# Kernel tuning notes

Hardware: AMD Instinct MI355X
Metric: run time of the kernel (lower is better)

Reference implementation:

```python
import jax, jax.numpy as jnp
import numpy as np

B, S, D_MODEL = 2, 2048, 512
KEY_DIM, VALUE_DIM, OUTPUT_DIM, NUM_HEADS = 256, 256, 512, 8


def setup_inputs() -> dict:
    key = jax.random.key(0)
    ks = jax.random.split(key, 12)
    s = 0.02
    return {
        "V": jax.random.normal(ks[0], (B, S, D_MODEL), jnp.float32),
        "Q": jax.random.normal(ks[1], (B, S, D_MODEL), jnp.float32),
        "K": jax.random.normal(ks[2], (B, S, D_MODEL), jnp.float32),
        "mask": jax.random.normal(ks[3], (B, 1, S, S), jnp.float32),
        "Wq": jax.random.normal(ks[4], (D_MODEL, KEY_DIM), jnp.float32) * s,
        "bq": jnp.zeros((KEY_DIM,), jnp.float32),
        "Wk": jax.random.normal(ks[5], (D_MODEL, KEY_DIM), jnp.float32) * s,
        "bk": jnp.zeros((KEY_DIM,), jnp.float32),
        "Wv": jax.random.normal(ks[6], (D_MODEL, VALUE_DIM), jnp.float32) * s,
        "bv": jnp.zeros((VALUE_DIM,), jnp.float32),
        "Wo": jax.random.normal(ks[7], (VALUE_DIM, OUTPUT_DIM), jnp.float32) * s,
        "bo": jnp.zeros((OUTPUT_DIM,), jnp.float32),
    }


def _split_heads(x, num_heads):
    # [B, S, H*d] -> [B, H, S, d]
    b, s, hd = x.shape
    return x.reshape(b, s, num_heads, hd // num_heads).transpose(0, 2, 1, 3)


def reference(V, Q, K, mask, Wq, bq, Wk, bk, Wv, bv, Wo, bo):
    denom = jnp.sqrt(jnp.float32(KEY_DIM))  # NOTE: full key_dim, as in source
    q = _split_heads(Q @ Wq + bq, NUM_HEADS)  # [B,H,S,dk]
    k = _split_heads(K @ Wk + bk, NUM_HEADS)
    scores = jnp.einsum("bhqd,bhkd->bhqk", q, k) / denom
    scores = scores + mask  # soft (additive) mask
    weights = jax.nn.softmax(scores, axis=-1)
    v = _split_heads(V @ Wv + bv, NUM_HEADS)  # [B,H,S,dv]
    ctx = jnp.einsum("bhqk,bhkd->bhqd", weights, v)  # [B,H,S,dv]
    b, h, s, d = ctx.shape
    ctx = ctx.transpose(0, 2, 1, 3).reshape(b, s, h * d)  # merge heads
    return ctx @ Wo + bo
```

## Files before the change

kernel.cpp:

```cpp
#include <hip/hip_runtime.h>

typedef __attribute__((ext_vector_type(8))) short bf16x8;
typedef __attribute__((ext_vector_type(4))) float f32x4;
typedef __attribute__((ext_vector_type(16))) float f32x16;

#define B_  2
#define S_  2048
#define DM  512
#define KD  256
#define HD  32
#define NH  8

__device__ __forceinline__ float bf2f(ushort u) {
    return __uint_as_float(((uint)u) << 16);
}
__device__ __forceinline__ ushort f2bf(float f) {
    uint x = __float_as_uint(f);
    return (ushort)((x + 0x7fffu + ((x >> 16) & 1u)) >> 16);
}
__device__ __forceinline__ uint cvt_pk_bf16(float lo, float hi) {
    uint r;
    asm("v_cvt_pk_bf16_f32 %0, %1, %2" : "=v"(r) : "v"(lo), "v"(hi));
    return r;
}
#define MFMA __builtin_amdgcn_mfma_f32_16x16x32_bf16
#define MFMA32 __builtin_amdgcn_mfma_f32_32x32x16_bf16

__device__ __forceinline__ int detect_isbf(const ushort* __restrict__ q)
{
    int lane = threadIdx.x & 63;
    int e = (q[lane] >> 7) & 0xFF;
    unsigned long long m = __ballot(e >= 100 && e <= 133);
    return __popcll(m) >= 58;
}

__global__ __launch_bounds__(256) void transpose_w(
    const void* __restrict__ Wq, const void* __restrict__ Wk, const void* __restrict__ Wv,
    const void* __restrict__ Wo,
    const void* __restrict__ bq, const void* __restrict__ bk,
    const void* __restrict__ bv, const void* __restrict__ bo,
    const ushort* __restrict__ qsrc,
    ushort* __restrict__ Wt, ushort* __restrict__ Wot, float* __restrict__ biasf)
{
    int isbf = detect_isbf(qsrc);
    int bid = blockIdx.x;
    if (bid >= 512) {
        for (int i = threadIdx.x; i < 1280; i += 256) {
            const void* bp; int off;
            if (i < 256)      { bp = bq; off = i; }
            else if (i < 512) { bp = bk; off = i - 256; }
            else if (i < 768) { bp = bv; off = i - 512; }
            else              { bp = bo; off = i - 768; }
            biasf[i] = isbf ? bf2f(((const ushort*)bp)[off]) : ((const float*)bp)[off];
        }
        return;
    }
    const void* W; int R, C; ushort* T;
    int m = bid >> 7, tix = bid & 127;
    if (m < 3) { W = (m == 0) ? Wq : (m == 1) ? Wk : Wv; R = 512; C = 256; T = Wt + m * 131072; }
    else       { W = Wo; R = 256; C = 512; T = Wot; }
    int tilesPerRow = C >> 5;
    int r0 = (tix / tilesPerRow) * 32, c0 = (tix % tilesPerRow) * 32;
    __shared__ float lds[32][33];
    int t = threadIdx.x;
    int rr = t >> 3, cc = (t & 7) * 4;
    if (isbf) {
        const ushort* Ws = (const ushort*)W;
        #pragma unroll
        for (int j = 0; j < 4; ++j) lds[rr][cc + j] = bf2f(Ws[(size_t)(r0 + rr) * C + c0 + cc + j]);
    } else {
        float4 v = *(const float4*)((const float*)W + (size_t)(r0 + rr) * C + c0 + cc);
        lds[rr][cc + 0] = v.x; lds[rr][cc + 1] = v.y; lds[rr][cc + 2] = v.z; lds[rr][cc + 3] = v.w;
    }
    __syncthreads();
    ushort4 o;
    o.x = f2bf(lds[cc + 0][rr]); o.y = f2bf(lds[cc + 1][rr]);
    o.z = f2bf(lds[cc + 2][rr]); o.w = f2bf(lds[cc + 3][rr]);
    int n = c0 + rr, k = r0 + cc;
    *(ushort4*)(T + ((((size_t)(n >> 4) * (R >> 3) + (k >> 3)) * 16 + (n & 15)) << 3) + (k & 7)) = o;
}

__global__ __launch_bounds__(256) void qkv_gemm(
    const void* __restrict__ Q, const void* __restrict__ K, const void* __restrict__ V,
    const ushort* __restrict__ Wt, const float* __restrict__ biasf,
    ushort* __restrict__ qh, ushort* __restrict__ kh, ushort* __restrict__ vT)
{
    int isbf = detect_isbf((const ushort*)Q);
    int y = blockIdx.y;
    const void* X = (y == 0) ? Q : (y == 1) ? K : V;
    int wave = threadIdx.x >> 6, lane = threadIdx.x & 63;
    int l16 = lane & 15, quad = lane >> 4;
    int m0 = blockIdx.x * 16;
    int n0 = wave * 64;
    const ushort* W = Wt + (size_t)y * (256 * 512);

    auto loadA = [&](int ks, bf16x8* a) {
        if (isbf) {
            *a = *(const bf16x8*)((const ushort*)X + (size_t)(m0 + l16) * 512 + ks + quad * 8);
        } else {
            const float* p = (const float*)X + (size_t)(m0 + l16) * 512 + ks + quad * 8;
            float4 f0 = *(const float4*)p, f1 = *(const float4*)(p + 4);
            union { uint u[4]; bf16x8 v; } cv;
            cv.u[0] = cvt_pk_bf16(f0.x, f0.y);
            cv.u[1] = cvt_pk_bf16(f0.z, f0.w);
            cv.u[2] = cvt_pk_bf16(f1.x, f1.y);
            cv.u[3] = cvt_pk_bf16(f1.z, f1.w);
            *a = cv.v;
        }
    };
    auto loadB = [&](int ks, bf16x8* b) {
        #pragma unroll
        for (int j = 0; j < 4; ++j)
            b[j] = *(const bf16x8*)(W + (((size_t)((n0 >> 4) + j) * 64 + (ks >> 3) + quad) * 16 + l16) * 8);
    };

    f32x4 acc[4] = {};
    bf16x8 aC, bC[4], aN, bN[4];
    loadA(0, &aC); loadB(0, bC);
    for (int ks = 0; ks < 512; ks += 32) {
        if (ks + 32 < 512) { loadA(ks + 32, &aN); loadB(ks + 32, bN); }
        #pragma unroll
        for (int j = 0; j < 4; ++j)
            acc[j] = MFMA(aC, bC[j], acc[j], 0, 0, 0);
        aC = aN;
        #pragma unroll
        for (int j = 0; j < 4; ++j) bC[j] = bN[j];
    }
    if (y < 2) {
        ushort* out = (y == 0) ? qh : kh;
        #pragma unroll
        for (int j = 0; j < 4; ++j) {
            int n = n0 + 16 * j + l16;
            float bs = biasf[y * 256 + n];
            int h = n >> 5, d = n & 31;
            #pragma unroll
            for (int r = 0; r < 4; ++r) {
                int rg = m0 + quad * 4 + r;
                int bb = rg >> 11, ss = rg & 2047;
                out[((((size_t)bb * NH + h) * S_ + ss) << 5) + d] = f2bf(acc[j][r] + bs);
            }
        }
    } else {
        int rg0 = m0 + quad * 4;
        int bb = rg0 >> 11, s0 = rg0 & 2047;
        #pragma unroll
        for (int j = 0; j < 4; ++j) {
            int n = n0 + 16 * j + l16;
            float bs = biasf[2 * 256 + n];
            int h = n >> 5, d = n & 31;
            ushort4 o;
            o.x = f2bf(acc[j][0] + bs); o.y = f2bf(acc[j][1] + bs);
            o.z = f2bf(acc[j][2] + bs); o.w = f2bf(acc[j][3] + bs);
            *(ushort4*)(vT + (((size_t)(bb * NH + h) * HD + d) * S_) + s0) = o;
        }
    }
}

__global__ __launch_bounds__(256) void attn(
    const ushort* __restrict__ qh, const ushort* __restrict__ kh,
    const ushort* __restrict__ vT, const void* __restrict__ maskp,
    float* __restrict__ pO, float* __restrict__ pl)
{
    __shared__ float ldsM[4][2][32][33];
    int isbf;
    {
        int lane = threadIdx.x & 63;
        ushort u = ((const ushort*)maskp)[lane];
        int e = (u >> 7) & 0xFF;
        unsigned long long m = __ballot(e >= 100 && e <= 133);
        isbf = __popcll(m) >= 58;
    }
    int wave = threadIdx.x >> 6, lane = threadIdx.x & 63;
    int l31 = lane & 31, hi = lane >> 5;
    int wid = blockIdx.x * 4 + wave;
    int chunk = wid & 1, qt32 = (wid >> 1) & 63, bh = wid >> 7;
    int b = bh >> 3;
    int q0 = qt32 * 32;
    const ushort* qb = qh + (size_t)bh * S_ * HD;
    const ushort* kb = kh + (size_t)bh * S_ * HD;
    const ushort* vb = vT + (size_t)bh * HD * S_;
    const ushort* mbb = (const ushort*)maskp + (size_t)b * S_ * S_;
    const float*  mbf = (const float*)maskp  + (size_t)b * S_ * S_;

    bf16x8 bq0 = *(const bf16x8*)(qb + (size_t)(q0 + l31) * HD + hi * 8);
    bf16x8 bq1 = *(const bf16x8*)(qb + (size_t)(q0 + l31) * HD + 16 + hi * 8);

    f32x16 O = {0,0,0,0,0,0,0,0,0,0,0,0,0,0,0,0};
    const f32x16 Z = {0,0,0,0,0,0,0,0,0,0,0,0,0,0,0,0};
    float lsum = 0.0f;

    int srow = (lane >> 3) & 7, scol = (lane & 7) * 4;
    float4 g[4];

    auto loadMg = [&](int k0) {
        if (isbf) {
            #pragma unroll
            for (int i = 0; i < 4; ++i) {
                ushort4 u = *(const ushort4*)(mbb + (size_t)(q0 + i * 8 + srow) * S_ + k0 + scol);
                float4 f; f.x = bf2f(u.x); f.y = bf2f(u.y); f.z = bf2f(u.z); f.w = bf2f(u.w);
                g[i] = f;
            }
        } else {
            #pragma unroll
            for (int i = 0; i < 4; ++i)
                g[i] = *(const float4*)(mbf + (size_t)(q0 + i * 8 + srow) * S_ + k0 + scol);
        }
    };
    auto writeM = [&](int buf) {
        #pragma unroll
        for (int i = 0; i < 4; ++i) {
            ldsM[wave][buf][i * 8 + srow][scol + 0] = g[i].x;
            ldsM[wave][buf][i * 8 + srow][scol + 1] = g[i].y;
            ldsM[wave][buf][i * 8 + srow][scol + 2] = g[i].z;
            ldsM[wave][buf][i * 8 + srow][scol + 3] = g[i].w;
        }
    };
    auto loadK = [&](int k0, bf16x8* K2) {
        K2[0] = *(const bf16x8*)(kb + (size_t)(k0 + l31) * HD + hi * 8);
        K2[1] = *(const bf16x8*)(kb + (size_t)(k0 + l31) * HD + 16 + hi * 8);
    };
    auto loadV = [&](int k0, bf16x8* V2) {
        V2[0] = *(const bf16x8*)(vb + (size_t)l31 * S_ + k0 + hi * 8);
        V2[1] = *(const bf16x8*)(vb + (size_t)l31 * S_ + k0 + 16 + hi * 8);
    };

    int kbase = chunk * 1024;

    auto sub = [&](int buf, bf16x8* Kc, bf16x8* Vc, bf16x8* Kn, bf16x8* Vn, int t) {
        float Mreg[16];
        #pragma unroll
        for (int r = 0; r < 16; ++r)
            Mreg[r] = ldsM[wave][buf][l31][(r & 3) + ((r >> 2) << 3) + (hi << 2)];
        int ktn = kbase + ((t + 1 < 32) ? (t + 1) : 31) * 32;
        loadK(ktn, Kn); loadV(ktn, Vn);
        f32x16 S = MFMA32(Kc[0], bq0, Z, 0, 0, 0);
        S = MFMA32(Kc[1], bq1, S, 0, 0, 0);
        writeM(buf ^ 1);
        int ktn2 = kbase + ((t + 2 < 32) ? (t + 2) : 31) * 32;
        loadMg(ktn2);
        float p[16];
        #pragma unroll
        for (int r = 0; r < 16; ++r) {
            p[r] = __expf(fmaf(S[r], 0.0625f, Mreg[r]));
            lsum += p[r];
        }
        union { uint u[4]; bf16x8 v; } pa0, pa1;
        {
            uint u0 = cvt_pk_bf16(p[0], p[1]),  w0 = cvt_pk_bf16(p[4], p[5]);
            uint u1 = cvt_pk_bf16(p[2], p[3]),  w1 = cvt_pk_bf16(p[6], p[7]);
            asm volatile("v_permlane32_swap_b32 %0, %1" : "+v"(u0), "+v"(w0));
            asm volatile("v_permlane32_swap_b32 %0, %1" : "+v"(u1), "+v"(w1));
            pa0.u[0] = u0; pa0.u[1] = u1; pa0.u[2] = w0; pa0.u[3] = w1;
            uint u2 = cvt_pk_bf16(p[8], p[9]),   w2 = cvt_pk_bf16(p[12], p[13]);
            uint u3 = cvt_pk_bf16(p[10], p[11]), w3 = cvt_pk_bf16(p[14], p[15]);
            asm volatile("v_permlane32_swap_b32 %0, %1" : "+v"(u2), "+v"(w2));
            asm volatile("v_permlane32_swap_b32 %0, %1" : "+v"(u3), "+v"(w3));
            pa1.u[0] = u2; pa1.u[1] = u3; pa1.u[2] = w2; pa1.u[3] = w3;
        }
        O = MFMA32(pa0.v, Vc[0], O, 0, 0, 0);
        O = MFMA32(pa1.v, Vc[1], O, 0, 0, 0);
    };

    bf16x8 KA[2], VA[2], KB[2], VB[2];
    loadK(kbase, KA); loadV(kbase, VA);
    loadMg(kbase); writeM(0);
    loadMg(kbase + 32);
    for (int t = 0; t < 32; t += 2) {
        sub(0, KA, VA, KB, VB, t);
        sub(1, KB, VB, KA, VA, t + 1);
    }

    float tot = lsum + __shfl_xor(lsum, 32, 64);
    int wid16_0 = ((bh * 128) + qt32 * 2 + 0) * 2 + chunk;
    int wid16_1 = ((bh * 128) + qt32 * 2 + 1) * 2 + chunk;
    if (lane < 32) {
        int q = l31;
        int w16 = (q < 16) ? wid16_0 : wid16_1;
        pl[w16 * 16 + (q & 15)] = tot;
    }
    #pragma unroll
    for (int r = 0; r < 16; ++r) {
        int q = (r & 3) + ((r >> 2) << 3) + (hi << 2);
        int w16 = (q < 16) ? wid16_0 : wid16_1;
        pO[(size_t)w16 * 512 + (q & 15) * 32 + l31] = O[r];
    }
}

__global__ __launch_bounds__(256) void out_proj(
    const float* __restrict__ pO, const float* __restrict__ pl,
    const ushort* __restrict__ Wot, const float* __restrict__ biasf,
    float* __restrict__ out)
{
    int wave = threadIdx.x >> 6, lane = threadIdx.x & 63;
    int l16 = lane & 15, quad = lane >> 4;
    int m0 = (blockIdx.x >> 1) * 16;
    int n0 = (blockIdx.x & 1) * 256 + wave * 64;
    f32x4 acc[4] = {};
    for (int ks = 0; ks < 256; ks += 32) {
        int h = ks >> 5;
        bf16x8 a, b[4];
        {
            int row = m0 + l16;
            int bb = row >> 11, s = row & 2047;
            int qt = s >> 4, r16 = s & 15;
            int wid0 = ((bb * NH + h) << 8) | (qt << 1);
            const float* p0 = pO + (size_t)wid0 * 512 + r16 * 32 + quad * 8;
            float4 x0 = *(const float4*)p0,         x1 = *(const float4*)(p0 + 4);
            float4 y0 = *(const float4*)(p0 + 512), y1 = *(const float4*)(p0 + 516);
            float il = 1.0f / (pl[wid0 * 16 + r16] + pl[(wid0 + 1) * 16 + r16]);
            union { uint u[4]; bf16x8 v; } cv;
            cv.u[0] = cvt_pk_bf16((x0.x + y0.x) * il, (x0.y + y0.y) * il);
            cv.u[1] = cvt_pk_bf16((x0.z + y0.z) * il, (x0.w + y0.w) * il);
            cv.u[2] = cvt_pk_bf16((x1.x + y1.x) * il, (x1.y + y1.y) * il);
            cv.u[3] = cvt_pk_bf16((x1.z + y1.z) * il, (x1.w + y1.w) * il);
            a = cv.v;
        }
        #pragma unroll
        for (int j = 0; j < 4; ++j)
            b[j] = *(const bf16x8*)(Wot + (((size_t)((n0 >> 4) + j) * 32 + (ks >> 3) + quad) * 16 + l16) * 8);
        #pragma unroll
        for (int j = 0; j < 4; ++j)
            acc[j] = MFMA(a, b[j], acc[j], 0, 0, 0);
    }
    #pragma unroll
    for (int j = 0; j < 4; ++j) {
        int n = n0 + 16 * j + l16;
        float bs = biasf[768 + n];
        #pragma unroll
        for (int r = 0; r < 4; ++r) {
            int rg = m0 + quad * 4 + r;
            out[(size_t)rg * DM + n] = acc[j][r] + bs;
        }
    }
}

extern "C" void kernel_launch(void* const* d_in, const int* in_sizes, int n_in,
                              void* d_out, int out_size, void* d_ws, size_t ws_size,
                              hipStream_t stream)
{
    const void* V    = d_in[0];
    const void* Q    = d_in[1];
    const void* K    = d_in[2];
    const void* mask = d_in[3];
    const void* Wq = d_in[4];  const void* bq = d_in[5];
    const void* Wk = d_in[6];  const void* bk = d_in[7];
    const void* Wv = d_in[8];  const void* bv = d_in[9];
    const void* Wo = d_in[10]; const void* bo = d_in[11];
    float* out = (float*)d_out;

    char* ws = (char*)d_ws;
    float*  biasf = (float*)ws;
    ushort* Wt  = (ushort*)(ws + 8192);
    ushort* Wot = Wt  + 393216;
    ushort* qh  = Wot + 131072;
    ushort* kh  = qh  + 1048576;
    ushort* vT  = kh  + 1048576;
    float*  pO  = (float*)(vT + 1048576);
    float*  pl  = pO + 4096 * 512;

    transpose_w<<<513, 256, 0, stream>>>(Wq, Wk, Wv, Wo, bq, bk, bv, bo,
                                         (const ushort*)Q, Wt, Wot, biasf);
    qkv_gemm<<<dim3(256, 3), 256, 0, stream>>>(Q, K, V, Wt, biasf, qh, kh, vT);
    attn<<<512, 256, 0, stream>>>(qh, kh, vT, mask, pO, pl);
    out_proj<<<512, 256, 0, stream>>>(pO, pl, Wot, biasf, out);
}
```

Before: 183.3 us.

## Process 64-key tiles per attention step and tile V for coalesced fragment loads

The attention inner loop now handles 64 keys per iteration instead of 32, issuing two score MFMAs pairs and four PV MFMAs per step with 64-wide mask tiles staged in LDS. The V projection output is rewritten into a tiled layout so each lane loads its bf16x8 V fragment from contiguous memory. The aim is to halve loop overhead and per-step latency exposure and to make V loads coalesced. In exchange it uses more registers and twice the LDS, which may lower occupancy.

```diff
diff --git a/kernel.cpp b/kernel.cpp
--- a/kernel.cpp
+++ b/kernel.cpp
@@ -142,7 +142,10 @@
         }
     } else {
         int rg0 = m0 + quad * 4;
-        int bb = rg0 >> 11, s0 = rg0 & 2047;
+        int bb = rg0 >> 11;
+        int tt = (rg0 & 2047) >> 4;
+        int sb = quad >> 1;
+        int jb = (quad & 1) * 4;
         #pragma unroll
         for (int j = 0; j < 4; ++j) {
             int n = n0 + 16 * j + l16;
@@ -151,7 +154,7 @@
             ushort4 o;
             o.x = f2bf(acc[j][0] + bs); o.y = f2bf(acc[j][1] + bs);
             o.z = f2bf(acc[j][2] + bs); o.w = f2bf(acc[j][3] + bs);
-            *(ushort4*)(vT + (((size_t)(bb * NH + h) * HD + d) * S_) + s0) = o;
+            *(ushort4*)(vT + ((((size_t)(bb * NH + h) * 128 + tt) * 64 + d + 32 * sb) << 3) + jb) = o;
         }
     }
 }
@@ -161,7 +164,7 @@
     const ushort* __restrict__ vT, const void* __restrict__ maskp,
     float* __restrict__ pO, float* __restrict__ pl)
 {
-    __shared__ float ldsM[4][2][32][33];
+    __shared__ float ldsM[4][2][32][66];
     int isbf;
     {
         int lane = threadIdx.x & 63;
@@ -178,7 +181,7 @@
     int q0 = qt32 * 32;
     const ushort* qb = qh + (size_t)bh * S_ * HD;
     const ushort* kb = kh + (size_t)bh * S_ * HD;
-    const ushort* vb = vT + (size_t)bh * HD * S_;
+    const ushort* vbp = vT + (size_t)bh * 65536;
     const ushort* mbb = (const ushort*)maskp + (size_t)b * S_ * S_;
     const float*  mbf = (const float*)maskp  + (size_t)b * S_ * S_;
 
@@ -189,83 +192,106 @@
     const f32x16 Z = {0,0,0,0,0,0,0,0,0,0,0,0,0,0,0,0};
     float lsum = 0.0f;
 
-    int srow = (lane >> 3) & 7, scol = (lane & 7) * 4;
-    float4 g[4];
+    int srow = lane >> 4;
+    int scol = (lane & 15) * 4;
+    float4 g[8];
 
     auto loadMg = [&](int k0) {
         if (isbf) {
             #pragma unroll
-            for (int i = 0; i < 4; ++i) {
-                ushort4 u = *(const ushort4*)(mbb + (size_t)(q0 + i * 8 + srow) * S_ + k0 + scol);
+            for (int i = 0; i < 8; ++i) {
+                ushort4 u = *(const ushort4*)(mbb + (size_t)(q0 + i * 4 + srow) * S_ + k0 + scol);
                 float4 f; f.x = bf2f(u.x); f.y = bf2f(u.y); f.z = bf2f(u.z); f.w = bf2f(u.w);
                 g[i] = f;
             }
         } else {
             #pragma unroll
-            for (int i = 0; i < 4; ++i)
-                g[i] = *(const float4*)(mbf + (size_t)(q0 + i * 8 + srow) * S_ + k0 + scol);
+            for (int i = 0; i < 8; ++i)
+                g[i] = *(const float4*)(mbf + (size_t)(q0 + i * 4 + srow) * S_ + k0 + scol);
         }
     };
     auto writeM = [&](int buf) {
         #pragma unroll
-        for (int i = 0; i < 4; ++i) {
-            ldsM[wave][buf][i * 8 + srow][scol + 0] = g[i].x;
-            ldsM[wave][buf][i * 8 + srow][scol + 1] = g[i].y;
-            ldsM[wave][buf][i * 8 + srow][scol + 2] = g[i].z;
-            ldsM[wave][buf][i * 8 + srow][scol + 3] = g[i].w;
-        }
-    };
-    auto loadK = [&](int k0, bf16x8* K2) {
-        K2[0] = *(const bf16x8*)(kb + (size_t)(k0 + l31) * HD + hi * 8);
-        K2[1] = *(const bf16x8*)(kb + (size_t)(k0 + l31) * HD + 16 + hi * 8);
-    };
-    auto loadV = [&](int k0, bf16x8* V2) {
-        V2[0] = *(const bf16x8*)(vb + (size_t)l31 * S_ + k0 + hi * 8);
-        V2[1] = *(const bf16x8*)(vb + (size_t)l31 * S_ + k0 + 16 + hi * 8);
+        for (int i = 0; i < 8; ++i) {
+            ldsM[wave][buf][i * 4 + srow][scol + 0] = g[i].x;
+            ldsM[wave][buf][i * 4 + srow][scol + 1] = g[i].y;
+            ldsM[wave][buf][i * 4 + srow][scol + 2] = g[i].z;
+            ldsM[wave][buf][i * 4 + srow][scol + 3] = g[i].w;
+        }
+    };
+    auto loadK = [&](int k0, bf16x8* K4) {
+        K4[0] = *(const bf16x8*)(kb + (size_t)(k0 + l31) * HD + hi * 8);
+        K4[1] = *(const bf16x8*)(kb + (size_t)(k0 + l31) * HD + 16 + hi * 8);
+        K4[2] = *(const bf16x8*)(kb + (size_t)(k0 + 32 + l31) * HD + hi * 8);
+        K4[3] = *(const bf16x8*)(kb + (size_t)(k0 + 32 + l31) * HD + 16 + hi * 8);
+    };
+    auto loadV = [&](int k0, bf16x8* V4) {
+        int t0 = k0 >> 4;
+        #pragma unroll
+        for (int i = 0; i < 4; ++i)
+            V4[i] = *(const bf16x8*)(vbp + (((size_t)(t0 + i) * 64 + lane) << 3));
     };
 
     int kbase = chunk * 1024;
 
     auto sub = [&](int buf, bf16x8* Kc, bf16x8* Vc, bf16x8* Kn, bf16x8* Vn, int t) {
-        float Mreg[16];
-        #pragma unroll
-        for (int r = 0; r < 16; ++r)
-            Mreg[r] = ldsM[wave][buf][l31][(r & 3) + ((r >> 2) << 3) + (hi << 2)];
-        int ktn = kbase + ((t + 1 < 32) ? (t + 1) : 31) * 32;
+        int ktn = kbase + ((t + 1 < 16) ? (t + 1) : 15) * 64;
         loadK(ktn, Kn); loadV(ktn, Vn);
-        f32x16 S = MFMA32(Kc[0], bq0, Z, 0, 0, 0);
-        S = MFMA32(Kc[1], bq1, S, 0, 0, 0);
+        float Mr0[16], Mr1[16];
+        #pragma unroll
+        for (int r = 0; r < 16; ++r) {
+            int c = (r & 3) + ((r >> 2) << 3) + (hi << 2);
+            Mr0[r] = ldsM[wave][buf][l31][c];
+            Mr1[r] = ldsM[wave][buf][l31][32 + c];
+        }
+        f32x16 S0 = MFMA32(Kc[0], bq0, Z, 0, 0, 0);
+        S0 = MFMA32(Kc[1], bq1, S0, 0, 0, 0);
+        f32x16 S1 = MFMA32(Kc[2], bq0, Z, 0, 0, 0);
+        S1 = MFMA32(Kc[3], bq1, S1, 0, 0, 0);
         writeM(buf ^ 1);
-        int ktn2 = kbase + ((t + 2 < 32) ? (t + 2) : 31) * 32;
-        loadMg(ktn2);
-        float p[16];
+        int ktm = kbase + ((t + 2 < 16) ? (t + 2) : 15) * 64;
+        loadMg(ktm);
         #pragma unroll
         for (int r = 0; r < 16; ++r) {
-            p[r] = __expf(fmaf(S[r], 0.0625f, Mreg[r]));
-            lsum += p[r];
-        }
-        union { uint u[4]; bf16x8 v; } pa0, pa1;
+            S0[r] = __expf(fmaf(S0[r], 0.0625f, Mr0[r]));
+            lsum += S0[r];
+            S1[r] = __expf(fmaf(S1[r], 0.0625f, Mr1[r]));
+            lsum += S1[r];
+        }
+        union { uint u[4]; bf16x8 v; } pa0, pa1, pa2, pa3;
         {
-            uint u0 = cvt_pk_bf16(p[0], p[1]),  w0 = cvt_pk_bf16(p[4], p[5]);
-            uint u1 = cvt_pk_bf16(p[2], p[3]),  w1 = cvt_pk_bf16(p[6], p[7]);
+            uint u0 = cvt_pk_bf16(S0[0], S0[1]),  w0 = cvt_pk_bf16(S0[4], S0[5]);
+            uint u1 = cvt_pk_bf16(S0[2], S0[3]),  w1 = cvt_pk_bf16(S0[6], S0[7]);
             asm volatile("v_permlane32_swap_b32 %0, %1" : "+v"(u0), "+v"(w0));
             asm volatile("v_permlane32_swap_b32 %0, %1" : "+v"(u1), "+v"(w1));
             pa0.u[0] = u0; pa0.u[1] = u1; pa0.u[2] = w0; pa0.u[3] = w1;
-            uint u2 = cvt_pk_bf16(p[8], p[9]),   w2 = cvt_pk_bf16(p[12], p[13]);
-            uint u3 = cvt_pk_bf16(p[10], p[11]), w3 = cvt_pk_bf16(p[14], p[15]);
+            uint u2 = cvt_pk_bf16(S0[8], S0[9]),   w2 = cvt_pk_bf16(S0[12], S0[13]);
+            uint u3 = cvt_pk_bf16(S0[10], S0[11]), w3 = cvt_pk_bf16(S0[14], S0[15]);
             asm volatile("v_permlane32_swap_b32 %0, %1" : "+v"(u2), "+v"(w2));
             asm volatile("v_permlane32_swap_b32 %0, %1" : "+v"(u3), "+v"(w3));
             pa1.u[0] = u2; pa1.u[1] = u3; pa1.u[2] = w2; pa1.u[3] = w3;
+            uint u4 = cvt_pk_bf16(S1[0], S1[1]),  w4 = cvt_pk_bf16(S1[4], S1[5]);
+            uint u5 = cvt_pk_bf16(S1[2], S1[3]),  w5 = cvt_pk_bf16(S1[6], S1[7]);
+            asm volatile("v_permlane32_swap_b32 %0, %1" : "+v"(u4), "+v"(w4));
+            asm volatile("v_permlane32_swap_b32 %0, %1" : "+v"(u5), "+v"(w5));
+            pa2.u[0] = u4; pa2.u[1] = u5; pa2.u[2] = w4; pa2.u[3] = w5;
+            uint u6 = cvt_pk_bf16(S1[8], S1[9]),   w6 = cvt_pk_bf16(S1[12], S1[13]);
+            uint u7 = cvt_pk_bf16(S1[10], S1[11]), w7 = cvt_pk_bf16(S1[14], S1[15]);
+            asm volatile("v_permlane32_swap_b32 %0, %1" : "+v"(u6), "+v"(w6));
+            asm volatile("v_permlane32_swap_b32 %0, %1" : "+v"(u7), "+v"(w7));
+            pa3.u[0] = u6; pa3.u[1] = u7; pa3.u[2] = w6; pa3.u[3] = w7;
         }
         O = MFMA32(pa0.v, Vc[0], O, 0, 0, 0);
         O = MFMA32(pa1.v, Vc[1], O, 0, 0, 0);
-    };
-
-    bf16x8 KA[2], VA[2], KB[2], VB[2];
+        O = MFMA32(pa2.v, Vc[2], O, 0, 0, 0);
+        O = MFMA32(pa3.v, Vc[3], O, 0, 0, 0);
+    };
+
+    bf16x8 KA[4], VA[4], KB[4], VB[4];
     loadK(kbase, KA); loadV(kbase, VA);
     loadMg(kbase); writeM(0);
-    loadMg(kbase + 32);
-    for (int t = 0; t < 32; t += 2) {
+    loadMg(kbase + 64);
+    for (int t = 0; t < 16; t += 2) {
         sub(0, KA, VA, KB, VB, t);
         sub(1, KB, VB, KA, VA, t + 1);
     }
```

Measured after the change: 177.3 us. -3.3%, faster.

## Share mask tiles across heads in one attention block and retile V layout

Applied to the files above, without the earlier changes.

The attention kernel now runs 512 threads per block, with one wave per head. All eight heads share a single LDS mask tile, so the head-independent additive mask is read from global memory once per block instead of once per head. V is written by the projection kernel in a tiled layout so each wave reads its MFMA operands with contiguous per-lane loads. The key-dimension split becomes configurable (four chunks when the workspace is large enough), and out_proj reduces across a variable number of partials. In exchange, every sub-step now needs a block-wide barrier, which couples the eight head waves together.

```diff
diff --git a/kernel.cpp b/kernel.cpp
--- a/kernel.cpp
+++ b/kernel.cpp
@@ -142,7 +142,10 @@
         }
     } else {
         int rg0 = m0 + quad * 4;
-        int bb = rg0 >> 11, s0 = rg0 & 2047;
+        int bb = rg0 >> 11;
+        int tt = (rg0 & 2047) >> 4;
+        int sb = quad >> 1;
+        int jb = (quad & 1) * 4;
         #pragma unroll
         for (int j = 0; j < 4; ++j) {
             int n = n0 + 16 * j + l16;
@@ -151,17 +154,17 @@
             ushort4 o;
             o.x = f2bf(acc[j][0] + bs); o.y = f2bf(acc[j][1] + bs);
             o.z = f2bf(acc[j][2] + bs); o.w = f2bf(acc[j][3] + bs);
-            *(ushort4*)(vT + (((size_t)(bb * NH + h) * HD + d) * S_) + s0) = o;
-        }
-    }
-}
-
-__global__ __launch_bounds__(256) void attn(
+            *(ushort4*)(vT + ((((size_t)(bb * NH + h) * 128 + tt) * 64 + d + 32 * sb) << 3) + jb) = o;
+        }
+    }
+}
+
+__global__ __launch_bounds__(512) void attn(
     const ushort* __restrict__ qh, const ushort* __restrict__ kh,
     const ushort* __restrict__ vT, const void* __restrict__ maskp,
-    float* __restrict__ pO, float* __restrict__ pl)
-{
-    __shared__ float ldsM[4][2][32][33];
+    float* __restrict__ pO, float* __restrict__ pl, int chsh)
+{
+    __shared__ float ldsM[2][32][33];
     int isbf;
     {
         int lane = threadIdx.x & 63;
@@ -170,15 +173,24 @@
         unsigned long long m = __ballot(e >= 100 && e <= 133);
         isbf = __popcll(m) >= 58;
     }
-    int wave = threadIdx.x >> 6, lane = threadIdx.x & 63;
+    int tid = threadIdx.x;
+    int wave = tid >> 6, lane = tid & 63;
     int l31 = lane & 31, hi = lane >> 5;
-    int wid = blockIdx.x * 4 + wave;
-    int chunk = wid & 1, qt32 = (wid >> 1) & 63, bh = wid >> 7;
-    int b = bh >> 3;
+    int CH = 1 << chsh;
+    int bid = blockIdx.x;
+    int chunk = bid & (CH - 1);
+    int qt32 = (bid >> chsh) & 63;
+    int b = bid >> (chsh + 6);
+    int h = wave;
+    int bh = b * NH + h;
     int q0 = qt32 * 32;
+    int klen = 2048 >> chsh;
+    int kbase = chunk * klen;
+    int NT = klen >> 5;
+
     const ushort* qb = qh + (size_t)bh * S_ * HD;
     const ushort* kb = kh + (size_t)bh * S_ * HD;
-    const ushort* vb = vT + (size_t)bh * HD * S_;
+    const ushort* vbp = vT + (size_t)bh * 65536;
     const ushort* mbb = (const ushort*)maskp + (size_t)b * S_ * S_;
     const float*  mbf = (const float*)maskp  + (size_t)b * S_ * S_;
 
@@ -189,55 +201,42 @@
     const f32x16 Z = {0,0,0,0,0,0,0,0,0,0,0,0,0,0,0,0};
     float lsum = 0.0f;
 
-    int srow = (lane >> 3) & 7, scol = (lane & 7) * 4;
-    float4 g[4];
+    int srow = tid >> 4, scol = (tid & 15) * 2;
+    float2 g;
 
     auto loadMg = [&](int k0) {
         if (isbf) {
-            #pragma unroll
-            for (int i = 0; i < 4; ++i) {
-                ushort4 u = *(const ushort4*)(mbb + (size_t)(q0 + i * 8 + srow) * S_ + k0 + scol);
-                float4 f; f.x = bf2f(u.x); f.y = bf2f(u.y); f.z = bf2f(u.z); f.w = bf2f(u.w);
-                g[i] = f;
-            }
+            ushort2 u = *(const ushort2*)(mbb + (size_t)(q0 + srow) * S_ + k0 + scol);
+            g.x = bf2f(u.x); g.y = bf2f(u.y);
         } else {
-            #pragma unroll
-            for (int i = 0; i < 4; ++i)
-                g[i] = *(const float4*)(mbf + (size_t)(q0 + i * 8 + srow) * S_ + k0 + scol);
+            g = *(const float2*)(mbf + (size_t)(q0 + srow) * S_ + k0 + scol);
         }
     };
     auto writeM = [&](int buf) {
-        #pragma unroll
-        for (int i = 0; i < 4; ++i) {
-            ldsM[wave][buf][i * 8 + srow][scol + 0] = g[i].x;
-            ldsM[wave][buf][i * 8 + srow][scol + 1] = g[i].y;
-            ldsM[wave][buf][i * 8 + srow][scol + 2] = g[i].z;
-            ldsM[wave][buf][i * 8 + srow][scol + 3] = g[i].w;
-        }
+        ldsM[buf][srow][scol]     = g.x;
+        ldsM[buf][srow][scol + 1] = g.y;
     };
     auto loadK = [&](int k0, bf16x8* K2) {
         K2[0] = *(const bf16x8*)(kb + (size_t)(k0 + l31) * HD + hi * 8);
         K2[1] = *(const bf16x8*)(kb + (size_t)(k0 + l31) * HD + 16 + hi * 8);
     };
     auto loadV = [&](int k0, bf16x8* V2) {
-        V2[0] = *(const bf16x8*)(vb + (size_t)l31 * S_ + k0 + hi * 8);
-        V2[1] = *(const bf16x8*)(vb + (size_t)l31 * S_ + k0 + 16 + hi * 8);
-    };
-
-    int kbase = chunk * 1024;
+        int t0 = k0 >> 4;
+        V2[0] = *(const bf16x8*)(vbp + (((size_t)t0 * 64 + lane) << 3));
+        V2[1] = *(const bf16x8*)(vbp + (((size_t)(t0 + 1) * 64 + lane) << 3));
+    };
 
     auto sub = [&](int buf, bf16x8* Kc, bf16x8* Vc, bf16x8* Kn, bf16x8* Vn, int t) {
         float Mreg[16];
         #pragma unroll
         for (int r = 0; r < 16; ++r)
-            Mreg[r] = ldsM[wave][buf][l31][(r & 3) + ((r >> 2) << 3) + (hi << 2)];
-        int ktn = kbase + ((t + 1 < 32) ? (t + 1) : 31) * 32;
+            Mreg[r] = ldsM[buf][l31][(r & 3) + ((r >> 2) << 3) + (hi << 2)];
+        int ktn = kbase + ((t + 1 < NT) ? (t + 1) : (NT - 1)) * 32;
         loadK(ktn, Kn); loadV(ktn, Vn);
         f32x16 S = MFMA32(Kc[0], bq0, Z, 0, 0, 0);
         S = MFMA32(Kc[1], bq1, S, 0, 0, 0);
         writeM(buf ^ 1);
-        int ktn2 = kbase + ((t + 2 < 32) ? (t + 2) : 31) * 32;
-        loadMg(ktn2);
+        loadMg(kbase + ((t + 2 < NT) ? (t + 2) : (NT - 1)) * 32);
         float p[16];
         #pragma unroll
         for (int r = 0; r < 16; ++r) {
@@ -259,20 +258,22 @@
         }
         O = MFMA32(pa0.v, Vc[0], O, 0, 0, 0);
         O = MFMA32(pa1.v, Vc[1], O, 0, 0, 0);
+        __syncthreads();
     };
 
     bf16x8 KA[2], VA[2], KB[2], VB[2];
     loadK(kbase, KA); loadV(kbase, VA);
     loadMg(kbase); writeM(0);
-    loadMg(kbase + 32);
-    for (int t = 0; t < 32; t += 2) {
+    loadMg(kbase + ((1 < NT) ? 32 : 0));
+    __syncthreads();
+    for (int t = 0; t < NT; t += 2) {
         sub(0, KA, VA, KB, VB, t);
         sub(1, KB, VB, KA, VA, t + 1);
     }
 
     float tot = lsum + __shfl_xor(lsum, 32, 64);
-    int wid16_0 = ((bh * 128) + qt32 * 2 + 0) * 2 + chunk;
-    int wid16_1 = ((bh * 128) + qt32 * 2 + 1) * 2 + chunk;
+    int wid16_0 = (((bh << 7) + qt32 * 2 + 0) << chsh) + chunk;
+    int wid16_1 = (((bh << 7) + qt32 * 2 + 1) << chsh) + chunk;
     if (lane < 32) {
         int q = l31;
         int w16 = (q < 16) ? wid16_0 : wid16_1;
@@ -289,12 +290,13 @@
 __global__ __launch_bounds__(256) void out_proj(
     const float* __restrict__ pO, const float* __restrict__ pl,
     const ushort* __restrict__ Wot, const float* __restrict__ biasf,
-    float* __restrict__ out)
+    float* __restrict__ out, int chsh)
 {
     int wave = threadIdx.x >> 6, lane = threadIdx.x & 63;
     int l16 = lane & 15, quad = lane >> 4;
     int m0 = (blockIdx.x >> 1) * 16;
     int n0 = (blockIdx.x & 1) * 256 + wave * 64;
+    int CH = 1 << chsh;
     f32x4 acc[4] = {};
     for (int ks = 0; ks < 256; ks += 32) {
         int h = ks >> 5;
@@ -303,16 +305,22 @@
             int row = m0 + l16;
             int bb = row >> 11, s = row & 2047;
             int qt = s >> 4, r16 = s & 15;
-            int wid0 = ((bb * NH + h) << 8) | (qt << 1);
-            const float* p0 = pO + (size_t)wid0 * 512 + r16 * 32 + quad * 8;
-            float4 x0 = *(const float4*)p0,         x1 = *(const float4*)(p0 + 4);
-            float4 y0 = *(const float4*)(p0 + 512), y1 = *(const float4*)(p0 + 516);
-            float il = 1.0f / (pl[wid0 * 16 + r16] + pl[(wid0 + 1) * 16 + r16]);
+            int wid0 = (((bb * NH + h) << 7) + qt) << chsh;
+            float s8[8] = {0, 0, 0, 0, 0, 0, 0, 0};
+            float lacc = 0.0f;
+            for (int cc = 0; cc < CH; ++cc) {
+                const float* p = pO + ((size_t)(wid0 + cc) << 9) + r16 * 32 + quad * 8;
+                float4 u0 = *(const float4*)p, u1 = *(const float4*)(p + 4);
+                s8[0] += u0.x; s8[1] += u0.y; s8[2] += u0.z; s8[3] += u0.w;
+                s8[4] += u1.x; s8[5] += u1.y; s8[6] += u1.z; s8[7] += u1.w;
+                lacc += pl[(wid0 + cc) * 16 + r16];
+            }
+            float il = 1.0f / lacc;
             union { uint u[4]; bf16x8 v; } cv;
-            cv.u[0] = cvt_pk_bf16((x0.x + y0.x) * il, (x0.y + y0.y) * il);
-            cv.u[1] = cvt_pk_bf16((x0.z + y0.z) * il, (x0.w + y0.w) * il);
-            cv.u[2] = cvt_pk_bf16((x1.x + y1.x) * il, (x1.y + y1.y) * il);
-            cv.u[3] = cvt_pk_bf16((x1.z + y1.z) * il, (x1.w + y1.w) * il);
+            cv.u[0] = cvt_pk_bf16(s8[0] * il, s8[1] * il);
+            cv.u[1] = cvt_pk_bf16(s8[2] * il, s8[3] * il);
+            cv.u[2] = cvt_pk_bf16(s8[4] * il, s8[5] * il);
+            cv.u[3] = cvt_pk_bf16(s8[6] * il, s8[7] * il);
             a = cv.v;
         }
         #pragma unroll
@@ -356,11 +364,12 @@
     ushort* kh  = qh  + 1048576;
     ushort* vT  = kh  + 1048576;
     float*  pO  = (float*)(vT + 1048576);
-    float*  pl  = pO + 4096 * 512;
+    int chsh = (ws_size >= 24649728u) ? 2 : 1;
+    float*  pl  = pO + ((size_t)2048 << chsh) * 512;
 
     transpose_w<<<513, 256, 0, stream>>>(Wq, Wk, Wv, Wo, bq, bk, bv, bo,
                                          (const ushort*)Q, Wt, Wot, biasf);
     qkv_gemm<<<dim3(256, 3), 256, 0, stream>>>(Q, K, V, Wt, biasf, qh, kh, vT);
-    attn<<<512, 256, 0, stream>>>(qh, kh, vT, mask, pO, pl);
-    out_proj<<<512, 256, 0, stream>>>(pO, pl, Wot, biasf, out);
-}
+    attn<<<128 << chsh, 512, 0, stream>>>(qh, kh, vT, mask, pO, pl, chsh);
+    out_proj<<<512, 256, 0, stream>>>(pO, pl, Wot, biasf, out, chsh);
+}
```

Measured after the change: 173.5 us. 5.4% less time.
